# Performance work log

Measured on AMD Instinct MI355X. Metric: run time of the kernel, lower is better.

## Reference

```python
import jax, jax.numpy as jnp
import numpy as np

L = 100  # hidden size of lstm1 (module hardcodes self.L = 100)


def _lstm_cell(x, h, c, W_ih, W_hh, b_ih, b_hh):
    # PyTorch LSTMCell: gates ordered (input, forget, cell, output)
    gates = x @ W_ih.T + h @ W_hh.T + b_ih + b_hh  # [B, 4*H]
    i, f, g, o = jnp.split(gates, 4, axis=-1)
    i = jax.nn.sigmoid(i)
    f = jax.nn.sigmoid(f)
    g = jnp.tanh(g)
    o = jax.nn.sigmoid(o)
    c_new = f * c + i * g
    h_new = o * jnp.tanh(c_new)
    return h_new, c_new


def setup_inputs() -> dict:
    key = jax.random.key(0)
    ks = jax.random.split(key, 9)
    B, T = 4096, 2048
    s1 = 1.0 / np.sqrt(L)   # torch LSTMCell init scale for hidden 100
    s2 = 1.0                # hidden size 1 -> scale 1
    return {
        "input": jax.random.normal(ks[0], (B, T), dtype=jnp.float32),
        "W_ih1": jax.random.uniform(ks[1], (4 * L, 1), jnp.float32, -s1, s1),
        "W_hh1": jax.random.uniform(ks[2], (4 * L, L), jnp.float32, -s1, s1),
        "b_ih1": jax.random.uniform(ks[3], (4 * L,), jnp.float32, -s1, s1),
        "b_hh1": jax.random.uniform(ks[4], (4 * L,), jnp.float32, -s1, s1),
        "W_ih2": jax.random.uniform(ks[5], (4, L), jnp.float32, -s2, s2),
        "W_hh2": jax.random.uniform(ks[6], (4, 1), jnp.float32, -s2, s2),
        "b_ih2": jax.random.uniform(ks[7], (4,), jnp.float32, -s2, s2),
        "b_hh2": jax.random.uniform(ks[8], (4,), jnp.float32, -s2, s2),
    }


def reference(input, W_ih1, W_hh1, b_ih1, b_hh1, W_ih2, W_hh2, b_ih2, b_hh2):
    B, T = input.shape
    x_seq = input.T[:, :, None]  # [T, B, 1]
    h1 = jnp.zeros((B, L), input.dtype)
    c1 = jnp.zeros((B, L), input.dtype)
    h2 = jnp.zeros((B, 1), input.dtype)
    c2 = jnp.zeros((B, 1), input.dtype)

    def step(carry, x_t):
        h1, c1, h2, c2 = carry
        h1, c1 = _lstm_cell(x_t, h1, c1, W_ih1, W_hh1, b_ih1, b_hh1)
        h2, c2 = _lstm_cell(h1, h2, c2, W_ih2, W_hh2, b_ih2, b_hh2)
        return (h1, c1, h2, c2), h2  # emit h2: [B, 1]

    _, outs = jax.lax.scan(step, (h1, c1, h2, c2), x_seq)
    # outs: [T, B, 1] -> stack along time dim then squeeze, matching torch.stack(.,1).squeeze(2)
    return outs[:, :, 0].T  # [B, T]
```

## Files before the change

kernel.cpp:

```cpp
#include <hip/hip_runtime.h>
#include <math.h>

#define BB 4096
#define TT 2048
#define LL 100

constexpr int NB = 16;
constexpr int WG = 448;

#define L2E 1.44269504088896340736f

#define AH(kt, row) (((kt) * 64 + ((row) ^ ((row) >> 3))) * 4)

typedef short bf16x8 __attribute__((ext_vector_type(8)));
typedef float f32x4 __attribute__((ext_vector_type(4)));

union AF { int4 v; bf16x8 f; unsigned int w[4]; };

__device__ __forceinline__ float frcp(float x) { return __builtin_amdgcn_rcpf(x); }
__device__ __forceinline__ float fexp2(float x) {
#if __has_builtin(__builtin_amdgcn_exp2f)
    return __builtin_amdgcn_exp2f(x);
#else
    return exp2f(x);
#endif
}
__device__ __forceinline__ float sig2(float xp) { return frcp(1.0f + fexp2(-xp)); }
__device__ __forceinline__ float th2(float xpp) { return 1.0f - 2.0f * frcp(1.0f + fexp2(xpp)); }
__device__ __forceinline__ float ftanh_n(float x) { return th2(2.0f * L2E * x); }

__device__ __forceinline__ unsigned int cvt_pk_bf16(float lo, float hi) {
    unsigned int d;
    asm("v_cvt_pk_bf16_f32 %0, %1, %2" : "=v"(d) : "v"(lo), "v"(hi));
    return d;
}

__global__ void __launch_bounds__(WG)
__attribute__((amdgpu_waves_per_eu(2, 2)))
lstm2_kernel(const float* __restrict__ input,
             const float* __restrict__ W_ih1,
             const float* __restrict__ W_hh1,
             const float* __restrict__ b_ih1,
             const float* __restrict__ b_hh1,
             const float* __restrict__ W_ih2,
             const float* __restrict__ W_hh2,
             const float* __restrict__ b_ih2,
             const float* __restrict__ b_hh2,
             float* __restrict__ out)
{
    __shared__ __align__(16) unsigned int afragH[2][1024];
    __shared__ __align__(16) unsigned int afragL[2][1024];

    const int tid = threadIdx.x;
    const int wave = tid >> 6;
    const int lane = tid & 63;
    const int col16 = lane & 15;
    const int quad = lane >> 4;
    const int bg0 = blockIdx.x * NB;

    for (int i = tid; i < 2 * 1024; i += WG) {
        (&afragH[0][0])[i] = 0u;
        (&afragL[0][0])[i] = 0u;
    }

    const int sb = (wave == 3) ? 6 : ((wave < 3) ? wave : wave - 1);
    const int uu = 16 * sb + col16;
    const bool uvalid = (uu < LL);
    const bool l2lane = (wave == 3) && (col16 == 8);
    const bool xlane = (wave == 3) && (col16 == 4);
    const bool wr_en = (uu <= 100);

    const float gsc[4] = {L2E, L2E, 2.0f * L2E, L2E};

    bf16x8 bhi[4][4], bmid[4][4];
#pragma unroll
    for (int g = 0; g < 4; ++g)
#pragma unroll
        for (int kt = 0; kt < 4; ++kt)
#pragma unroll
            for (int j = 0; j < 8; ++j) {
                const int k = 32 * kt + 8 * quad + j;
                float w = 0.0f;
                if (k < LL) {
                    if (l2lane)       w = W_ih2[g * LL + k] * gsc[g];
                    else if (uvalid)  w = W_hh1[(100 * g + uu) * LL + k] * gsc[g];
                } else if (k == 100) {
                    if (!l2lane && uvalid) w = W_ih1[100 * g + uu] * gsc[g];
                }
                const unsigned int hh = cvt_pk_bf16(w, 0.0f) & 0xffffu;
                bhi[g][kt][j] = (short)hh;
                const float wres = w - __uint_as_float(hh << 16);
                bmid[g][kt][j] = (short)(cvt_pk_bf16(wres, 0.0f) & 0xffffu);
            }

    f32x4 binit[4];
#pragma unroll
    for (int g = 0; g < 4; ++g) {
        float bv = 0.0f;
        if (l2lane)      bv = (b_ih2[g] + b_hh2[g]) * gsc[g];
        else if (uvalid) bv = (b_ih1[100 * g + uu] + b_hh1[100 * g + uu]) * gsc[g];
        binit[g] = (f32x4){bv, bv, bv, bv};
    }

    float c1[4] = {0.f, 0.f, 0.f, 0.f};

    const int kt_u = uu >> 5;
    const int lnb = ((uu >> 3) & 3) * 16;
    const int jh = (uu & 7) >> 1;
    const int hwo = uu & 1;

    float wh2s[4], h2v[4] = {0.f, 0.f, 0.f, 0.f}, c2v[4] = {0.f, 0.f, 0.f, 0.f};
#pragma unroll
    for (int g = 0; g < 4; ++g)
        wh2s[g] = l2lane ? W_hh2[g] * gsc[g] : 0.0f;

    __syncthreads();

    if (xlane) {
#pragma unroll
        for (int r = 0; r < 4; ++r) {
            const int m = 4 * quad + r;
            const float x0 = input[(size_t)(bg0 + m) * TT];
            const unsigned int hh = cvt_pk_bf16(x0, x0);
            const float hl = x0 - __uint_as_float(hh << 16);
            const unsigned int hlp = cvt_pk_bf16(hl, hl);
            const int hw = (AH(3, lnb + m) + jh) * 2 + hwo;
            ((short*)&afragH[0][0])[hw] = (short)hh;
            ((short*)&afragL[0][0])[hw] = (short)hlp;
        }
    }
    __syncthreads();

    for (int t = 0; t <= TT; ++t) {
        const int p = t & 1, pn = p ^ 1;

        if (t < TT || wave == 3) {
            float xnext[4] = {0.f, 0.f, 0.f, 0.f};
            if (xlane && t + 1 < TT) {
#pragma unroll
                for (int r = 0; r < 4; ++r)
                    xnext[r] = input[(size_t)(bg0 + 4 * quad + r) * TT + (t + 1)];
            }

            AF ahi[4];
#pragma unroll
            for (int kt = 0; kt < 4; ++kt)
                ahi[kt].v = *(const int4*)&afragH[p][AH(kt, lane)];

            f32x4 acc[4];
#pragma unroll
            for (int g = 0; g < 4; ++g)
                acc[g] = __builtin_amdgcn_mfma_f32_16x16x32_bf16(ahi[0].f, bhi[g][0], binit[g], 0, 0, 0);
#pragma unroll
            for (int kt = 1; kt < 4; ++kt)
#pragma unroll
                for (int g = 0; g < 4; ++g)
                    acc[g] = __builtin_amdgcn_mfma_f32_16x16x32_bf16(ahi[kt].f, bhi[g][kt], acc[g], 0, 0, 0);
#pragma unroll
            for (int kt = 0; kt < 4; ++kt)
#pragma unroll
                for (int g = 0; g < 4; ++g)
                    acc[g] = __builtin_amdgcn_mfma_f32_16x16x32_bf16(ahi[kt].f, bmid[g][kt], acc[g], 0, 0, 0);

            AF alo[4];
#pragma unroll
            for (int kt = 0; kt < 4; ++kt)
                alo[kt].v = *(const int4*)&afragL[p][AH(kt, lane)];
#pragma unroll
            for (int kt = 0; kt < 4; ++kt)
#pragma unroll
                for (int g = 0; g < 4; ++g)
                    acc[g] = __builtin_amdgcn_mfma_f32_16x16x32_bf16(alo[kt].f, bhi[g][kt], acc[g], 0, 0, 0);

            if (l2lane && t >= 1) {
#pragma unroll
                for (int r = 0; r < 4; ++r) {
                    const float p0 = fmaf(wh2s[0], h2v[r], acc[0][r]);
                    const float p1 = fmaf(wh2s[1], h2v[r], acc[1][r]);
                    const float p2 = fmaf(wh2s[2], h2v[r], acc[2][r]);
                    const float p3 = fmaf(wh2s[3], h2v[r], acc[3][r]);
                    const float i2 = sig2(p0), f2 = sig2(p1), g2 = th2(p2), o2 = sig2(p3);
                    c2v[r] = f2 * c2v[r] + i2 * g2;
                    h2v[r] = o2 * ftanh_n(c2v[r]);
                    out[(size_t)(bg0 + 4 * quad + r) * TT + (t - 1)] = h2v[r];
                }
            }

            if (t < TT) {
#pragma unroll
                for (int r = 0; r < 4; ++r) {
                    const int m = 4 * quad + r;
                    const float iv = sig2(acc[0][r]);
                    const float fv = sig2(acc[1][r]);
                    const float gv = th2(acc[2][r]);
                    const float ov = sig2(acc[3][r]);
                    const float c = fv * c1[r] + iv * gv;
                    c1[r] = c;
                    const float h = uvalid ? (ov * ftanh_n(c)) : xnext[r];
                    if (wr_en) {
                        const unsigned int hh = cvt_pk_bf16(h, h);
                        const float hl = h - __uint_as_float(hh << 16);
                        const unsigned int hlp = cvt_pk_bf16(hl, hl);
                        const int hw = (AH(kt_u, lnb + m) + jh) * 2 + hwo;
                        ((short*)&afragH[pn][0])[hw] = (short)hh;
                        ((short*)&afragL[pn][0])[hw] = (short)hlp;
                    }
                }
            }
        }

        __syncthreads();
    }
}

extern "C" void kernel_launch(void* const* d_in, const int* in_sizes, int n_in,
                              void* d_out, int out_size, void* d_ws, size_t ws_size,
                              hipStream_t stream) {
    const float* input = (const float*)d_in[0];
    const float* W_ih1 = (const float*)d_in[1];
    const float* W_hh1 = (const float*)d_in[2];
    const float* b_ih1 = (const float*)d_in[3];
    const float* b_hh1 = (const float*)d_in[4];
    const float* W_ih2 = (const float*)d_in[5];
    const float* W_hh2 = (const float*)d_in[6];
    const float* b_ih2 = (const float*)d_in[7];
    const float* b_hh2 = (const float*)d_in[8];
    float* out = (float*)d_out;

    dim3 grid(BB / NB);
    dim3 block(WG);
    lstm2_kernel<<<grid, block, 0, stream>>>(input, W_ih1, W_hh1, b_ih1, b_hh1,
                                             W_ih2, W_hh2, b_ih2, b_hh2, out);
}
```

Measured before the change: 2.783 ms.

## Interleave hi/lo bf16 split terms along K to cut MFMA count per step

The kernel used to keep separate hi and lo bf16 activation buffers and run three passes of MFMAs (hi·hi, hi·mid, lo·hi), 48 per step. It now packs each hidden value's hi and lo halves into adjacent K slots of one buffer, and pairs them with the weight's hi and residual halves. That cuts the work to 7 K-tiles × 4 gates = 28 MFMAs, with one packed 32-bit LDS store per value instead of two 16-bit stores. The trade-off is accuracy: the new pairing computes h_hi·w_hi + h_lo·w_res and drops the cross terms h_hi·w_mid and h_lo·w_hi. The result is close to plain bf16 precision, and errors could compound over the 2048-step recurrence.

```diff
diff --git a/kernel.cpp b/kernel.cpp
--- a/kernel.cpp
+++ b/kernel.cpp
@@ -7,10 +7,11 @@
 
 constexpr int NB = 16;
 constexpr int WG = 448;
+constexpr int KT = 7;
 
 #define L2E 1.44269504088896340736f
 
-#define AH(kt, row) (((kt) * 64 + ((row) ^ ((row) >> 3))) * 4)
+#define AG(kt, row) (((kt) * 64 + ((row) ^ ((row) >> 3))) * 4)
 
 typedef short bf16x8 __attribute__((ext_vector_type(8)));
 typedef float f32x4 __attribute__((ext_vector_type(4)));
@@ -48,8 +49,7 @@
              const float* __restrict__ b_hh2,
              float* __restrict__ out)
 {
-    __shared__ __align__(16) unsigned int afragH[2][1024];
-    __shared__ __align__(16) unsigned int afragL[2][1024];
+    __shared__ __align__(16) unsigned int afrag[2][KT * 256];
 
     const int tid = threadIdx.x;
     const int wave = tid >> 6;
@@ -58,10 +58,7 @@
     const int quad = lane >> 4;
     const int bg0 = blockIdx.x * NB;
 
-    for (int i = tid; i < 2 * 1024; i += WG) {
-        (&afragH[0][0])[i] = 0u;
-        (&afragL[0][0])[i] = 0u;
-    }
+    for (int i = tid; i < 2 * KT * 256; i += WG) (&afrag[0][0])[i] = 0u;
 
     const int sb = (wave == 3) ? 6 : ((wave < 3) ? wave : wave - 1);
     const int uu = 16 * sb + col16;
@@ -72,25 +69,29 @@
 
     const float gsc[4] = {L2E, L2E, 2.0f * L2E, L2E};
 
-    bf16x8 bhi[4][4], bmid[4][4];
+    bf16x8 bb[4][KT];
 #pragma unroll
     for (int g = 0; g < 4; ++g)
 #pragma unroll
-        for (int kt = 0; kt < 4; ++kt)
+        for (int kt = 0; kt < KT; ++kt)
 #pragma unroll
             for (int j = 0; j < 8; ++j) {
                 const int k = 32 * kt + 8 * quad + j;
+                const int i = k >> 1;
                 float w = 0.0f;
-                if (k < LL) {
-                    if (l2lane)       w = W_ih2[g * LL + k] * gsc[g];
-                    else if (uvalid)  w = W_hh1[(100 * g + uu) * LL + k] * gsc[g];
-                } else if (k == 100) {
+                if (i < LL) {
+                    if (l2lane)       w = W_ih2[g * LL + i] * gsc[g];
+                    else if (uvalid)  w = W_hh1[(100 * g + uu) * LL + i] * gsc[g];
+                } else if (i == 100) {
                     if (!l2lane && uvalid) w = W_ih1[100 * g + uu] * gsc[g];
                 }
                 const unsigned int hh = cvt_pk_bf16(w, 0.0f) & 0xffffu;
-                bhi[g][kt][j] = (short)hh;
-                const float wres = w - __uint_as_float(hh << 16);
-                bmid[g][kt][j] = (short)(cvt_pk_bf16(wres, 0.0f) & 0xffffu);
+                if (!(k & 1)) {
+                    bb[g][kt][j] = (short)hh;
+                } else {
+                    const float wres = w - __uint_as_float(hh << 16);
+                    bb[g][kt][j] = (short)(cvt_pk_bf16(wres, 0.0f) & 0xffffu);
+                }
             }
 
     f32x4 binit[4];
@@ -104,10 +105,12 @@
 
     float c1[4] = {0.f, 0.f, 0.f, 0.f};
 
-    const int kt_u = uu >> 5;
-    const int lnb = ((uu >> 3) & 3) * 16;
-    const int jh = (uu & 7) >> 1;
-    const int hwo = uu & 1;
+    int wofs[4];
+#pragma unroll
+    for (int r = 0; r < 4; ++r) {
+        const int row = 4 * quad + r + 16 * ((col16 >> 2) & 3);
+        wofs[r] = AG(sb, row) + (col16 & 3);
+    }
 
     float wh2s[4], h2v[4] = {0.f, 0.f, 0.f, 0.f}, c2v[4] = {0.f, 0.f, 0.f, 0.f};
 #pragma unroll
@@ -122,11 +125,8 @@
             const int m = 4 * quad + r;
             const float x0 = input[(size_t)(bg0 + m) * TT];
             const unsigned int hh = cvt_pk_bf16(x0, x0);
-            const float hl = x0 - __uint_as_float(hh << 16);
-            const unsigned int hlp = cvt_pk_bf16(hl, hl);
-            const int hw = (AH(3, lnb + m) + jh) * 2 + hwo;
-            ((short*)&afragH[0][0])[hw] = (short)hh;
-            ((short*)&afragL[0][0])[hw] = (short)hlp;
+            const float hf = __uint_as_float(hh << 16);
+            afrag[0][wofs[r]] = cvt_pk_bf16(x0, x0 - hf);
         }
     }
     __syncthreads();
@@ -142,35 +142,20 @@
                     xnext[r] = input[(size_t)(bg0 + 4 * quad + r) * TT + (t + 1)];
             }
 
-            AF ahi[4];
-#pragma unroll
-            for (int kt = 0; kt < 4; ++kt)
-                ahi[kt].v = *(const int4*)&afragH[p][AH(kt, lane)];
+            AF a[KT];
+#pragma unroll
+            for (int kt = 0; kt < KT; ++kt)
+                a[kt].v = *(const int4*)&afrag[p][AG(kt, lane)];
 
             f32x4 acc[4];
 #pragma unroll
             for (int g = 0; g < 4; ++g)
-                acc[g] = __builtin_amdgcn_mfma_f32_16x16x32_bf16(ahi[0].f, bhi[g][0], binit[g], 0, 0, 0);
-#pragma unroll
-            for (int kt = 1; kt < 4; ++kt)
+                acc[g] = __builtin_amdgcn_mfma_f32_16x16x32_bf16(a[0].f, bb[g][0], binit[g], 0, 0, 0);
+#pragma unroll
+            for (int kt = 1; kt < KT; ++kt)
 #pragma unroll
                 for (int g = 0; g < 4; ++g)
-                    acc[g] = __builtin_amdgcn_mfma_f32_16x16x32_bf16(ahi[kt].f, bhi[g][kt], acc[g], 0, 0, 0);
-#pragma unroll
-            for (int kt = 0; kt < 4; ++kt)
-#pragma unroll
-                for (int g = 0; g < 4; ++g)
-                    acc[g] = __builtin_amdgcn_mfma_f32_16x16x32_bf16(ahi[kt].f, bmid[g][kt], acc[g], 0, 0, 0);
-
-            AF alo[4];
-#pragma unroll
-            for (int kt = 0; kt < 4; ++kt)
-                alo[kt].v = *(const int4*)&afragL[p][AH(kt, lane)];
-#pragma unroll
-            for (int kt = 0; kt < 4; ++kt)
-#pragma unroll
-                for (int g = 0; g < 4; ++g)
-                    acc[g] = __builtin_amdgcn_mfma_f32_16x16x32_bf16(alo[kt].f, bhi[g][kt], acc[g], 0, 0, 0);
+                    acc[g] = __builtin_amdgcn_mfma_f32_16x16x32_bf16(a[kt].f, bb[g][kt], acc[g], 0, 0, 0);
 
             if (l2lane && t >= 1) {
 #pragma unroll
@@ -189,7 +174,6 @@
             if (t < TT) {
 #pragma unroll
                 for (int r = 0; r < 4; ++r) {
-                    const int m = 4 * quad + r;
                     const float iv = sig2(acc[0][r]);
                     const float fv = sig2(acc[1][r]);
                     const float gv = th2(acc[2][r]);
@@ -199,11 +183,8 @@
                     const float h = uvalid ? (ov * ftanh_n(c)) : xnext[r];
                     if (wr_en) {
                         const unsigned int hh = cvt_pk_bf16(h, h);
-                        const float hl = h - __uint_as_float(hh << 16);
-                        const unsigned int hlp = cvt_pk_bf16(hl, hl);
-                        const int hw = (AH(kt_u, lnb + m) + jh) * 2 + hwo;
-                        ((short*)&afragH[pn][0])[hw] = (short)hh;
-                        ((short*)&afragL[pn][0])[hw] = (short)hlp;
+                        const float hf = __uint_as_float(hh << 16);
+                        afrag[pn][wofs[r]] = cvt_pk_bf16(h, h - hf);
                     }
                 }
             }
```

Result: faster. 2.322 ms (-16.5%).
